# Kernel optimization log

Measured on AMD Instinct MI355X. Metric: run time of the kernel, lower is better.

The kernel has to match this reference:

```python
import jax, jax.numpy as jnp
import numpy as np

D_MODEL = 768
H = 12
D_K = D_MODEL // H
B = 2
S = 2048
NEG = -1e9


def setup_inputs() -> dict:
    key = jax.random.key(0)
    ks = jax.random.split(key, 12)
    scale = 1.0 / np.sqrt(D_MODEL)
    inp = {
        "q": jax.random.normal(ks[0], (B, S, D_MODEL), jnp.float32),
        "k": jax.random.normal(ks[1], (B, S, D_MODEL), jnp.float32),
        "v": jax.random.normal(ks[2], (B, S, D_MODEL), jnp.float32),
        "mask": jax.random.randint(ks[3], (B, 1, S, S), 0, 2, jnp.int32),
        "Wq": jax.random.normal(ks[4], (D_MODEL, D_MODEL), jnp.float32) * scale,
        "bq": jnp.zeros((D_MODEL,), jnp.float32),
        "Wk": jax.random.normal(ks[5], (D_MODEL, D_MODEL), jnp.float32) * scale,
        "bk": jnp.zeros((D_MODEL,), jnp.float32),
        "Wv": jax.random.normal(ks[6], (D_MODEL, D_MODEL), jnp.float32) * scale,
        "bv": jnp.zeros((D_MODEL,), jnp.float32),
        "Wo": jax.random.normal(ks[7], (D_MODEL, D_MODEL), jnp.float32) * scale,
        "bo": jnp.zeros((D_MODEL,), jnp.float32),
    }
    return inp


def _split_heads(x):
    # [B, S, D] -> [B, H, S, D_K]
    b, s, _ = x.shape
    return x.reshape(b, s, H, D_K).transpose(0, 2, 1, 3)


def reference(q, k, v, mask, Wq, bq, Wk, bk, Wv, bv, Wo, bo):
    # torch Linear: x @ W.T + b
    query = _split_heads(q @ Wq.T + bq)
    key_ = _split_heads(k @ Wk.T + bk)
    value = _split_heads(v @ Wv.T + bv)

    scores = jnp.einsum("bhqd,bhkd->bhqk", query, key_) / np.sqrt(D_K)
    scores = jnp.where(mask == 0, NEG, scores)
    attn = jax.nn.softmax(scores, axis=-1)  # dropout p=0.0 -> identity

    x = jnp.einsum("bhqk,bhkd->bhqd", attn, value)
    x = x.transpose(0, 2, 1, 3).reshape(q.shape[0], -1, D_MODEL)
    return x @ Wo.T + bo
```

## Files before the change

### kernel.cpp

```cpp
#include <hip/hip_runtime.h>
#include <math.h>

#define DMODEL 768
#define NHEAD 12
#define DKDIM 64
#define BB 2
#define SS 2048
#define MROWS (BB * SS)
#define WELEM (DMODEL * DMODEL)
#define MWORDS (SS / 64)
#define NIT (SS / 64)

typedef unsigned short bf16_t;
typedef __attribute__((ext_vector_type(8))) short s8;
typedef __attribute__((ext_vector_type(4))) float f4;

#define MFMA(a, b, c) __builtin_amdgcn_mfma_f32_16x16x32_bf16((a), (b), (c), 0, 0, 0)

__device__ __forceinline__ bf16_t f2bf(float f) {
    unsigned u = __float_as_uint(f);
    u += 0x7fffu + ((u >> 16) & 1u);
    return (bf16_t)(u >> 16);
}
__device__ __forceinline__ unsigned cvtpk2(float a, float b) {
    unsigned r;
    asm("v_cvt_pk_bf16_f32 %0, %1, %2" : "=v"(r) : "v"(a), "v"(b));
    return r;
}
__device__ __forceinline__ s8 ldfrag(const bf16_t* p) {
    union { uint4 u; s8 s; } x;
    x.u = *(const uint4*)p;
    return x.s;
}

__device__ __forceinline__ void ld_stage(const bf16_t* p, uint4& u0, uint4& u1) {
    u0 = *(const uint4*)p;
    u1 = *(const uint4*)(p + 8);
}
__device__ __forceinline__ void ld_stage(const float* p, uint4& u0, uint4& u1) {
    const float4 f0 = *(const float4*)p;
    const float4 f1 = *(const float4*)(p + 4);
    const float4 f2 = *(const float4*)(p + 8);
    const float4 f3 = *(const float4*)(p + 12);
    u0.x = cvtpk2(f0.x, f0.y); u0.y = cvtpk2(f0.z, f0.w);
    u0.z = cvtpk2(f1.x, f1.y); u0.w = cvtpk2(f1.z, f1.w);
    u1.x = cvtpk2(f2.x, f2.y); u1.y = cvtpk2(f2.z, f2.w);
    u1.z = cvtpk2(f3.x, f3.y); u1.w = cvtpk2(f3.z, f3.w);
}

__global__ void cvt_weights(const float* __restrict__ W0, const float* __restrict__ W1,
                            const float* __restrict__ W2, const float* __restrict__ W3,
                            bf16_t* __restrict__ dst)
{
    const float* src = (blockIdx.y == 0) ? W0 : (blockIdx.y == 1) ? W1
                     : (blockIdx.y == 2) ? W2 : W3;
    bf16_t* d = dst + (size_t)blockIdx.y * WELEM;
    const int i = (blockIdx.x * 256 + threadIdx.x) * 4;
    const float4 v = *(const float4*)(src + i);
    uint2 h;
    h.x = cvtpk2(v.x, v.y);
    h.y = cvtpk2(v.z, v.w);
    *(uint2*)(d + i) = h;
}

__global__ __launch_bounds__(256) void mask_to_bits(
    const int* __restrict__ mask, unsigned long long* __restrict__ mbits)
{
    const size_t gid = (size_t)blockIdx.x * 256 + threadIdx.x;
    const int m = mask[gid];
    const unsigned long long bal = __ballot(m != 0);
    if ((threadIdx.x & 63) == 0) mbits[gid >> 6] = bal;
}

template<typename TA, typename TO>
__global__ __launch_bounds__(256) void gemm_tiled(
    const TA* __restrict__ A0, const TA* __restrict__ A1, const TA* __restrict__ A2,
    const bf16_t* __restrict__ W0, const bf16_t* __restrict__ W1, const bf16_t* __restrict__ W2,
    const float* __restrict__ bias0, const float* __restrict__ bias1, const float* __restrict__ bias2,
    TO* __restrict__ C0, TO* __restrict__ C1, TO* __restrict__ C2,
    float sc0, float sc1, float sc2)
{
    __shared__ uint4 As4[128 * 4];
    __shared__ uint4 Bs4[128 * 4];

    const int z = blockIdx.z;
    const TA*     A    = (z == 0) ? A0 : (z == 1) ? A1 : A2;
    const bf16_t* W    = (z == 0) ? W0 : (z == 1) ? W1 : W2;
    const float*  bias = (z == 0) ? bias0 : (z == 1) ? bias1 : bias2;
    TO*           C    = (z == 0) ? C0 : (z == 1) ? C1 : C2;
    const float   sc   = (z == 0) ? sc0 : (z == 1) ? sc1 : sc2;

    const int tid  = threadIdx.x;
    const int lane = tid & 63;
    const int w    = tid >> 6;
    const int wm   = w & 1;
    const int wn   = w >> 1;
    const int l15  = lane & 15;
    const int quad = lane >> 4;
    const int m0   = blockIdx.y * 128;
    const int n0   = blockIdx.x * 128;

    const int srow  = tid >> 1;
    const int shalf = tid & 1;
    const int sw    = srow & 3;

    const TA*     aptr = A + (size_t)(m0 + srow) * DMODEL + shalf * 16;
    const bf16_t* wptr = W + (size_t)(n0 + srow) * DMODEL + shalf * 16;

    f4 acc[4][4];
    #pragma unroll
    for (int i = 0; i < 4; i++)
        #pragma unroll
        for (int j = 0; j < 4; j++)
            acc[i][j] = (f4){0.f, 0.f, 0.f, 0.f};

    for (int k0 = 0; k0 < DMODEL; k0 += 32) {
        uint4 au0, au1, bu0, bu1;
        ld_stage(aptr + k0, au0, au1);
        ld_stage(wptr + k0, bu0, bu1);
        __syncthreads();
        As4[srow * 4 + ((shalf * 2 + 0) ^ sw)] = au0;
        As4[srow * 4 + ((shalf * 2 + 1) ^ sw)] = au1;
        Bs4[srow * 4 + ((shalf * 2 + 0) ^ sw)] = bu0;
        Bs4[srow * 4 + ((shalf * 2 + 1) ^ sw)] = bu1;
        __syncthreads();

        s8 af[4], bf[4];
        #pragma unroll
        for (int t = 0; t < 4; t++) {
            const int ar = wm * 64 + t * 16 + l15;
            const int br = wn * 64 + t * 16 + l15;
            union { uint4 u; s8 s; } xa, xb;
            xa.u = As4[ar * 4 + (quad ^ (ar & 3))];
            xb.u = Bs4[br * 4 + (quad ^ (br & 3))];
            af[t] = xa.s;
            bf[t] = xb.s;
        }
        #pragma unroll
        for (int mt = 0; mt < 4; mt++)
            #pragma unroll
            for (int nt = 0; nt < 4; nt++)
                acc[mt][nt] = MFMA(af[mt], bf[nt], acc[mt][nt]);
    }

    #pragma unroll
    for (int mt = 0; mt < 4; mt++) {
        #pragma unroll
        for (int nt = 0; nt < 4; nt++) {
            const int col = n0 + wn * 64 + nt * 16 + l15;
            const float bb = bias[col];
            #pragma unroll
            for (int reg = 0; reg < 4; reg++) {
                const int row = m0 + wm * 64 + mt * 16 + quad * 4 + reg;
                const float val = (acc[mt][nt][reg] + bb) * sc;
                TO* dst = C + (size_t)row * DMODEL + col;
                if constexpr (sizeof(TO) == 2) *dst = f2bf(val);
                else                           *dst = val;
            }
        }
    }
}

__global__ __launch_bounds__(256) void attn_mfma(
    const bf16_t* __restrict__ Q, const bf16_t* __restrict__ K,
    const bf16_t* __restrict__ V, const unsigned long long* __restrict__ mbits,
    bf16_t* __restrict__ O)
{
    __shared__ unsigned Vs[2][64][36];
    __shared__ unsigned Ps[4][16][36];

    const int tid  = threadIdx.x;
    const int lane = tid & 63;
    const int w    = tid >> 6;
    const int l15  = lane & 15;
    const int quad = lane >> 4;
    const int q0   = blockIdx.x * 64;
    const int h    = blockIdx.y;
    const int b    = blockIdx.z;
    const size_t base = ((size_t)b * SS) * DMODEL + (size_t)h * DKDIM;

    const bf16_t* qrow = Q + base + (size_t)(q0 + w * 16 + l15) * DMODEL + quad * 8;
    const s8 qf0 = ldfrag(qrow);
    const s8 qf1 = ldfrag(qrow + 32);

    f4 oacc[4];
    float l_part[4];
    #pragma unroll
    for (int i = 0; i < 4; i++) {
        oacc[i] = (f4){0.f, 0.f, 0.f, 0.f};
        l_part[i] = 0.0f;
    }

    const int kp  = tid & 31;
    const int oct = tid >> 5;
    const bf16_t* vbase = V + base + (size_t)(2 * kp) * DMODEL + oct * 8;
    const bf16_t* kbase = K + base + (size_t)l15 * DMODEL + quad * 8;

    const unsigned long long* mbase =
        mbits + ((size_t)b * SS + (q0 + w * 16 + quad * 4)) * MWORDS;

    uint4 va = *(const uint4*)(vbase);
    uint4 vb = *(const uint4*)(vbase + DMODEL);
    {
        const unsigned short* pa = (const unsigned short*)&va;
        const unsigned short* pb = (const unsigned short*)&vb;
        #pragma unroll
        for (int i = 0; i < 8; i++)
            Vs[0][oct * 8 + i][kp] = (unsigned)pa[i] | ((unsigned)pb[i] << 16);
    }
    va = *(const uint4*)(vbase + (size_t)64 * DMODEL);
    vb = *(const uint4*)(vbase + (size_t)64 * DMODEL + DMODEL);

    s8 kf0[4], kf1[4];
    unsigned long long mw[4];
    #pragma unroll
    for (int nt = 0; nt < 4; nt++) {
        const bf16_t* krow = kbase + (size_t)(nt * 16) * DMODEL;
        kf0[nt] = ldfrag(krow);
        kf1[nt] = ldfrag(krow + 32);
    }
    #pragma unroll
    for (int reg = 0; reg < 4; reg++)
        mw[reg] = mbase[(size_t)reg * MWORDS];

    __syncthreads();

    for (int it = 0; it < NIT; ++it) {
        const int k0  = it * 64;
        const int cur = it & 1;

        if (it + 1 < NIT) {
            const unsigned short* pa = (const unsigned short*)&va;
            const unsigned short* pb = (const unsigned short*)&vb;
            #pragma unroll
            for (int i = 0; i < 8; i++)
                Vs[cur ^ 1][oct * 8 + i][kp] = (unsigned)pa[i] | ((unsigned)pb[i] << 16);
            if (it + 2 < NIT) {
                va = *(const uint4*)(vbase + (size_t)(k0 + 128) * DMODEL);
                vb = *(const uint4*)(vbase + (size_t)(k0 + 128) * DMODEL + DMODEL);
            }
        }

        f4 sacc[4];
        __builtin_amdgcn_s_setprio(1);
        #pragma unroll
        for (int nt = 0; nt < 4; nt++) {
            f4 zz = {0.f, 0.f, 0.f, 0.f};
            zz = MFMA(qf0, kf0[nt], zz);
            zz = MFMA(qf1, kf1[nt], zz);
            sacc[nt] = zz;
        }
        __builtin_amdgcn_s_setprio(0);

        unsigned long long mwc[4];
        #pragma unroll
        for (int reg = 0; reg < 4; reg++) mwc[reg] = mw[reg];
        if (it + 1 < NIT) {
            #pragma unroll
            for (int nt = 0; nt < 4; nt++) {
                const bf16_t* krow = kbase + (size_t)(k0 + 64 + nt * 16) * DMODEL;
                kf0[nt] = ldfrag(krow);
                kf1[nt] = ldfrag(krow + 32);
            }
            #pragma unroll
            for (int reg = 0; reg < 4; reg++)
                mw[reg] = mbase[(size_t)reg * MWORDS + it + 1];
        }

        #pragma unroll
        for (int reg = 0; reg < 4; reg++) {
            const unsigned mlo = ((unsigned)mwc[reg]) >> l15;
            const unsigned mhi = ((unsigned)(mwc[reg] >> 32)) >> l15;
            float p[4];
            p[0] = (mlo & 1u)       ? __expf(sacc[0][reg]) : 0.0f;
            p[1] = (mlo & 0x10000u) ? __expf(sacc[1][reg]) : 0.0f;
            p[2] = (mhi & 1u)       ? __expf(sacc[2][reg]) : 0.0f;
            p[3] = (mhi & 0x10000u) ? __expf(sacc[3][reg]) : 0.0f;
            l_part[reg] += (p[0] + p[1]) + (p[2] + p[3]);

            #pragma unroll
            for (int nt = 0; nt < 4; nt++) {
                const float mine  = p[nt];
                const float other = __shfl_xor(mine, 1, 16);
                if ((lane & 1) == 0)
                    Ps[w][quad * 4 + reg][nt * 8 + (l15 >> 1)] = cvtpk2(mine, other);
            }
        }

        __builtin_amdgcn_s_setprio(1);
        #pragma unroll
        for (int kt = 0; kt < 2; kt++) {
            union { uint4 u; s8 s; } pf;
            pf.u = *(const uint4*)&Ps[w][l15][kt * 16 + quad * 4];
            #pragma unroll
            for (int dt = 0; dt < 4; dt++) {
                union { uint4 u; s8 s; } vf;
                vf.u = *(const uint4*)&Vs[cur][dt * 16 + l15][kt * 16 + quad * 4];
                oacc[dt] = MFMA(pf.s, vf.s, oacc[dt]);
            }
        }
        __builtin_amdgcn_s_setprio(0);

        __syncthreads();
    }

    #pragma unroll
    for (int reg = 0; reg < 4; reg++) {
        float rs = l_part[reg];
        rs += __shfl_xor(rs, 1, 16);
        rs += __shfl_xor(rs, 2, 16);
        rs += __shfl_xor(rs, 4, 16);
        rs += __shfl_xor(rs, 8, 16);
        const float inv = 1.0f / rs;
        const size_t row = q0 + w * 16 + quad * 4 + reg;
        #pragma unroll
        for (int dt = 0; dt < 4; dt++) {
            O[base + row * DMODEL + dt * 16 + l15] = f2bf(oacc[dt][reg] * inv);
        }
    }
}

extern "C" void kernel_launch(void* const* d_in, const int* in_sizes, int n_in,
                              void* d_out, int out_size, void* d_ws, size_t ws_size,
                              hipStream_t stream)
{
    const float* q    = (const float*)d_in[0];
    const float* k    = (const float*)d_in[1];
    const float* v    = (const float*)d_in[2];
    const int*   mask = (const int*)  d_in[3];
    const float* Wq   = (const float*)d_in[4];
    const float* bq   = (const float*)d_in[5];
    const float* Wk   = (const float*)d_in[6];
    const float* bk   = (const float*)d_in[7];
    const float* Wv   = (const float*)d_in[8];
    const float* bv   = (const float*)d_in[9];
    const float* Wo   = (const float*)d_in[10];
    const float* bo   = (const float*)d_in[11];
    float* out = (float*)d_out;

    bf16_t* wsb = (bf16_t*)d_ws;
    const size_t plane = (size_t)MROWS * DMODEL;
    bf16_t* Qp  = wsb;
    bf16_t* Kp  = wsb + plane;
    bf16_t* Vp  = wsb + 2 * plane;
    bf16_t* Ctx = wsb + 3 * plane;
    bf16_t* Wqb = wsb + 4 * plane;
    bf16_t* Wkb = Wqb + WELEM;
    bf16_t* Wvb = Wkb + WELEM;
    bf16_t* Wob = Wvb + WELEM;
    unsigned long long* mbits = (unsigned long long*)(Wob + WELEM);

    cvt_weights<<<dim3(WELEM / 1024, 4), 256, 0, stream>>>(Wq, Wk, Wv, Wo, Wqb);
    mask_to_bits<<<dim3((BB * SS * SS) / 256), 256, 0, stream>>>(mask, mbits);

    gemm_tiled<float, bf16_t><<<dim3(DMODEL / 128, MROWS / 128, 3), 256, 0, stream>>>(
        q, k, v, Wqb, Wkb, Wvb, bq, bk, bv, Qp, Kp, Vp, 0.125f, 1.0f, 1.0f);

    attn_mfma<<<dim3(SS / 64, NHEAD, BB), 256, 0, stream>>>(Qp, Kp, Vp, mbits, Ctx);

    gemm_tiled<bf16_t, float><<<dim3(DMODEL / 128, MROWS / 128, 1), 256, 0, stream>>>(
        Ctx, Ctx, Ctx, Wob, Wob, Wob, bo, bo, bo, out, out, out, 1.0f, 1.0f, 1.0f);
}
```

Baseline: 340.6 us.

## Use float additive mask, pre-convert inputs, and shuffle P fragments in registers

Replaces the packed mask bitfield with a full float additive-bias tensor that is fed in as the MFMA accumulator init. It also folds log2(e) into the Q scale so exp2 can be used, and transposes the QK^T product. The P fragments are now built with cross-lane shuffles instead of a shared-memory round trip. Inputs are converted to bf16 in a separate pass before the projection GEMM, and the row-sum reduction is simplified. The aim is to cut LDS traffic and masking ALU work, at the cost of writing a 32 MB float mask and re-reading it once per head instead of a compact bitmask.

```diff
diff --git a/kernel.cpp b/kernel.cpp
--- a/kernel.cpp
+++ b/kernel.cpp
@@ -8,7 +8,6 @@
 #define SS 2048
 #define MROWS (BB * SS)
 #define WELEM (DMODEL * DMODEL)
-#define MWORDS (SS / 64)
 #define NIT (SS / 64)
 
 typedef unsigned short bf16_t;
@@ -21,6 +20,9 @@
     unsigned u = __float_as_uint(f);
     u += 0x7fffu + ((u >> 16) & 1u);
     return (bf16_t)(u >> 16);
+}
+__device__ __forceinline__ unsigned pack2(float a, float b) {
+    return (unsigned)f2bf(a) | ((unsigned)f2bf(b) << 16);
 }
 __device__ __forceinline__ unsigned cvtpk2(float a, float b) {
     unsigned r;
@@ -42,10 +44,10 @@
     const float4 f1 = *(const float4*)(p + 4);
     const float4 f2 = *(const float4*)(p + 8);
     const float4 f3 = *(const float4*)(p + 12);
-    u0.x = cvtpk2(f0.x, f0.y); u0.y = cvtpk2(f0.z, f0.w);
-    u0.z = cvtpk2(f1.x, f1.y); u0.w = cvtpk2(f1.z, f1.w);
-    u1.x = cvtpk2(f2.x, f2.y); u1.y = cvtpk2(f2.z, f2.w);
-    u1.z = cvtpk2(f3.x, f3.y); u1.w = cvtpk2(f3.z, f3.w);
+    u0.x = pack2(f0.x, f0.y); u0.y = pack2(f0.z, f0.w);
+    u0.z = pack2(f1.x, f1.y); u0.w = pack2(f1.z, f1.w);
+    u1.x = pack2(f2.x, f2.y); u1.y = pack2(f2.z, f2.w);
+    u1.z = pack2(f3.x, f3.y); u1.w = pack2(f3.z, f3.w);
 }
 
 __global__ void cvt_weights(const float* __restrict__ W0, const float* __restrict__ W1,
@@ -57,19 +59,35 @@
     bf16_t* d = dst + (size_t)blockIdx.y * WELEM;
     const int i = (blockIdx.x * 256 + threadIdx.x) * 4;
     const float4 v = *(const float4*)(src + i);
-    uint2 h;
-    h.x = cvtpk2(v.x, v.y);
-    h.y = cvtpk2(v.z, v.w);
-    *(uint2*)(d + i) = h;
-}
-
-__global__ __launch_bounds__(256) void mask_to_bits(
-    const int* __restrict__ mask, unsigned long long* __restrict__ mbits)
-{
-    const size_t gid = (size_t)blockIdx.x * 256 + threadIdx.x;
-    const int m = mask[gid];
-    const unsigned long long bal = __ballot(m != 0);
-    if ((threadIdx.x & 63) == 0) mbits[gid >> 6] = bal;
+    ushort4 h;
+    h.x = f2bf(v.x); h.y = f2bf(v.y); h.z = f2bf(v.z); h.w = f2bf(v.w);
+    *(ushort4*)(d + i) = h;
+}
+
+__global__ __launch_bounds__(256) void cvt_inputs(
+    const float* __restrict__ A0, const float* __restrict__ A1,
+    const float* __restrict__ A2, bf16_t* __restrict__ dst)
+{
+    const float* src = (blockIdx.y == 0) ? A0 : (blockIdx.y == 1) ? A1 : A2;
+    bf16_t* d = dst + (size_t)blockIdx.y * MROWS * DMODEL;
+    const int i = (blockIdx.x * 256 + threadIdx.x) * 4;
+    const float4 v = *(const float4*)(src + i);
+    ushort4 h;
+    h.x = f2bf(v.x); h.y = f2bf(v.y); h.z = f2bf(v.z); h.w = f2bf(v.w);
+    *(ushort4*)(d + i) = h;
+}
+
+__global__ __launch_bounds__(256) void mask_to_bias(
+    const int* __restrict__ mask, float* __restrict__ fb)
+{
+    const size_t i = ((size_t)blockIdx.x * 256 + threadIdx.x) * 4;
+    const int4 m = *(const int4*)(mask + i);
+    float4 o;
+    o.x = m.x ? 0.0f : -1.0e9f;
+    o.y = m.y ? 0.0f : -1.0e9f;
+    o.z = m.z ? 0.0f : -1.0e9f;
+    o.w = m.w ? 0.0f : -1.0e9f;
+    *(float4*)(fb + i) = o;
 }
 
 template<typename TA, typename TO>
@@ -163,11 +181,10 @@
 
 __global__ __launch_bounds__(256) void attn_mfma(
     const bf16_t* __restrict__ Q, const bf16_t* __restrict__ K,
-    const bf16_t* __restrict__ V, const unsigned long long* __restrict__ mbits,
+    const bf16_t* __restrict__ V, const float* __restrict__ FB,
     bf16_t* __restrict__ O)
 {
     __shared__ unsigned Vs[2][64][36];
-    __shared__ unsigned Ps[4][16][36];
 
     const int tid  = threadIdx.x;
     const int lane = tid & 63;
@@ -184,20 +201,19 @@
     const s8 qf1 = ldfrag(qrow + 32);
 
     f4 oacc[4];
-    float l_part[4];
-    #pragma unroll
-    for (int i = 0; i < 4; i++) {
-        oacc[i] = (f4){0.f, 0.f, 0.f, 0.f};
-        l_part[i] = 0.0f;
-    }
+    #pragma unroll
+    for (int i = 0; i < 4; i++) oacc[i] = (f4){0.f, 0.f, 0.f, 0.f};
+    float l_part = 0.0f;
 
     const int kp  = tid & 31;
     const int oct = tid >> 5;
     const bf16_t* vbase = V + base + (size_t)(2 * kp) * DMODEL + oct * 8;
     const bf16_t* kbase = K + base + (size_t)l15 * DMODEL + quad * 8;
-
-    const unsigned long long* mbase =
-        mbits + ((size_t)b * SS + (q0 + w * 16 + quad * 4)) * MWORDS;
+    const float* fbrow = FB + ((size_t)b * SS + q0 + w * 16 + l15) * SS + quad * 4;
+
+    const int sA  = l15 + (((2 * quad) & 3) << 4);
+    const int sB  = l15 + (((2 * quad + 1) & 3) << 4);
+    const bool hiQ = (quad & 2) != 0;
 
     uint4 va = *(const uint4*)(vbase);
     uint4 vb = *(const uint4*)(vbase + DMODEL);
@@ -212,16 +228,14 @@
     vb = *(const uint4*)(vbase + (size_t)64 * DMODEL + DMODEL);
 
     s8 kf0[4], kf1[4];
-    unsigned long long mw[4];
+    f4 fb[4];
     #pragma unroll
     for (int nt = 0; nt < 4; nt++) {
         const bf16_t* krow = kbase + (size_t)(nt * 16) * DMODEL;
         kf0[nt] = ldfrag(krow);
         kf1[nt] = ldfrag(krow + 32);
-    }
-    #pragma unroll
-    for (int reg = 0; reg < 4; reg++)
-        mw[reg] = mbase[(size_t)reg * MWORDS];
+        fb[nt]  = *(const f4*)(fbrow + nt * 16);
+    }
 
     __syncthreads();
 
@@ -245,77 +259,75 @@
         __builtin_amdgcn_s_setprio(1);
         #pragma unroll
         for (int nt = 0; nt < 4; nt++) {
-            f4 zz = {0.f, 0.f, 0.f, 0.f};
-            zz = MFMA(qf0, kf0[nt], zz);
-            zz = MFMA(qf1, kf1[nt], zz);
+            f4 zz = fb[nt];
+            zz = MFMA(kf0[nt], qf0, zz);
+            zz = MFMA(kf1[nt], qf1, zz);
             sacc[nt] = zz;
         }
         __builtin_amdgcn_s_setprio(0);
 
-        unsigned long long mwc[4];
-        #pragma unroll
-        for (int reg = 0; reg < 4; reg++) mwc[reg] = mw[reg];
         if (it + 1 < NIT) {
             #pragma unroll
             for (int nt = 0; nt < 4; nt++) {
                 const bf16_t* krow = kbase + (size_t)(k0 + 64 + nt * 16) * DMODEL;
                 kf0[nt] = ldfrag(krow);
                 kf1[nt] = ldfrag(krow + 32);
+                fb[nt]  = *(const f4*)(fbrow + k0 + 64 + nt * 16);
             }
-            #pragma unroll
-            for (int reg = 0; reg < 4; reg++)
-                mw[reg] = mbase[(size_t)reg * MWORDS + it + 1];
-        }
-
-        #pragma unroll
-        for (int reg = 0; reg < 4; reg++) {
-            const unsigned mlo = ((unsigned)mwc[reg]) >> l15;
-            const unsigned mhi = ((unsigned)(mwc[reg] >> 32)) >> l15;
-            float p[4];
-            p[0] = (mlo & 1u)       ? __expf(sacc[0][reg]) : 0.0f;
-            p[1] = (mlo & 0x10000u) ? __expf(sacc[1][reg]) : 0.0f;
-            p[2] = (mhi & 1u)       ? __expf(sacc[2][reg]) : 0.0f;
-            p[3] = (mhi & 0x10000u) ? __expf(sacc[3][reg]) : 0.0f;
-            l_part[reg] += (p[0] + p[1]) + (p[2] + p[3]);
-
-            #pragma unroll
-            for (int nt = 0; nt < 4; nt++) {
-                const float mine  = p[nt];
-                const float other = __shfl_xor(mine, 1, 16);
-                if ((lane & 1) == 0)
-                    Ps[w][quad * 4 + reg][nt * 8 + (l15 >> 1)] = cvtpk2(mine, other);
-            }
-        }
-
-        __builtin_amdgcn_s_setprio(1);
+        }
+
+        unsigned w01[4], w23[4];
+        #pragma unroll
+        for (int nt = 0; nt < 4; nt++) {
+            const float p0 = __builtin_exp2f(sacc[nt][0]);
+            const float p1 = __builtin_exp2f(sacc[nt][1]);
+            const float p2 = __builtin_exp2f(sacc[nt][2]);
+            const float p3 = __builtin_exp2f(sacc[nt][3]);
+            l_part += (p0 + p1) + (p2 + p3);
+            w01[nt] = cvtpk2(p0, p1);
+            w23[nt] = cvtpk2(p2, p3);
+        }
+
         #pragma unroll
         for (int kt = 0; kt < 2; kt++) {
+            const unsigned a0 = (unsigned)__shfl((int)w01[2 * kt],     sA, 64);
+            const unsigned a1 = (unsigned)__shfl((int)w01[2 * kt + 1], sA, 64);
+            const unsigned b0 = (unsigned)__shfl((int)w23[2 * kt],     sA, 64);
+            const unsigned b1 = (unsigned)__shfl((int)w23[2 * kt + 1], sA, 64);
+            const unsigned c0 = (unsigned)__shfl((int)w01[2 * kt],     sB, 64);
+            const unsigned c1 = (unsigned)__shfl((int)w01[2 * kt + 1], sB, 64);
+            const unsigned d0 = (unsigned)__shfl((int)w23[2 * kt],     sB, 64);
+            const unsigned d1 = (unsigned)__shfl((int)w23[2 * kt + 1], sB, 64);
             union { uint4 u; s8 s; } pf;
-            pf.u = *(const uint4*)&Ps[w][l15][kt * 16 + quad * 4];
+            pf.u.x = hiQ ? a1 : a0;
+            pf.u.y = hiQ ? b1 : b0;
+            pf.u.z = hiQ ? c1 : c0;
+            pf.u.w = hiQ ? d1 : d0;
+
+            __builtin_amdgcn_s_setprio(1);
             #pragma unroll
             for (int dt = 0; dt < 4; dt++) {
                 union { uint4 u; s8 s; } vf;
                 vf.u = *(const uint4*)&Vs[cur][dt * 16 + l15][kt * 16 + quad * 4];
                 oacc[dt] = MFMA(pf.s, vf.s, oacc[dt]);
             }
-        }
-        __builtin_amdgcn_s_setprio(0);
+            __builtin_amdgcn_s_setprio(0);
+        }
 
         __syncthreads();
     }
 
+    l_part += __shfl_xor(l_part, 16, 64);
+    l_part += __shfl_xor(l_part, 32, 64);
+    const float inv = 1.0f / l_part;
+
     #pragma unroll
     for (int reg = 0; reg < 4; reg++) {
-        float rs = l_part[reg];
-        rs += __shfl_xor(rs, 1, 16);
-        rs += __shfl_xor(rs, 2, 16);
-        rs += __shfl_xor(rs, 4, 16);
-        rs += __shfl_xor(rs, 8, 16);
-        const float inv = 1.0f / rs;
+        const float invq = __shfl(inv, (quad << 4) + quad * 4 + reg, 64);
         const size_t row = q0 + w * 16 + quad * 4 + reg;
         #pragma unroll
         for (int dt = 0; dt < 4; dt++) {
-            O[base + row * DMODEL + dt * 16 + l15] = f2bf(oacc[dt][reg] * inv);
+            O[base + row * DMODEL + dt * 16 + l15] = f2bf(oacc[dt][reg] * invq);
         }
     }
 }
@@ -348,15 +360,19 @@
     bf16_t* Wkb = Wqb + WELEM;
     bf16_t* Wvb = Wkb + WELEM;
     bf16_t* Wob = Wvb + WELEM;
-    unsigned long long* mbits = (unsigned long long*)(Wob + WELEM);
+    bf16_t* Abf = Wob + WELEM;
+    float*  FB  = (float*)Abf;
 
     cvt_weights<<<dim3(WELEM / 1024, 4), 256, 0, stream>>>(Wq, Wk, Wv, Wo, Wqb);
-    mask_to_bits<<<dim3((BB * SS * SS) / 256), 256, 0, stream>>>(mask, mbits);
-
-    gemm_tiled<float, bf16_t><<<dim3(DMODEL / 128, MROWS / 128, 3), 256, 0, stream>>>(
-        q, k, v, Wqb, Wkb, Wvb, bq, bk, bv, Qp, Kp, Vp, 0.125f, 1.0f, 1.0f);
-
-    attn_mfma<<<dim3(SS / 64, NHEAD, BB), 256, 0, stream>>>(Qp, Kp, Vp, mbits, Ctx);
+    cvt_inputs<<<dim3((int)(plane / 1024), 3), 256, 0, stream>>>(q, k, v, Abf);
+
+    gemm_tiled<bf16_t, bf16_t><<<dim3(DMODEL / 128, MROWS / 128, 3), 256, 0, stream>>>(
+        Abf, Abf + plane, Abf + 2 * plane, Wqb, Wkb, Wvb, bq, bk, bv,
+        Qp, Kp, Vp, 0.125f * 1.44269504f, 1.0f, 1.0f);
+
+    mask_to_bias<<<dim3((BB * SS * SS) / 1024), 256, 0, stream>>>(mask, FB);
+
+    attn_mfma<<<dim3(SS / 64, NHEAD, BB), 256, 0, stream>>>(Qp, Kp, Vp, FB, Ctx);
 
     gemm_tiled<bf16_t, float><<<dim3(DMODEL / 128, MROWS / 128, 1), 256, 0, stream>>>(
         Ctx, Ctx, Ctx, Wob, Wob, Wob, bo, bo, bo, out, out, out, 1.0f, 1.0f, 1.0f);
```

Result: slower. 353.6 us (+3.8%).
